# Kernel tuning notes

Measured on AMD Instinct MI355X. Metric: run time of the kernel, lower is better.

## Reference

```python
import jax, jax.numpy as jnp
import numpy as np

TEMP = 0.07
W00 = 0.1
EPS = 1e-8


def setup_inputs() -> dict:
    key = jax.random.key(0)
    k1, k2, k3, k4 = jax.random.split(key, 4)
    B, N, D = 32, 256, 256
    M = B * N
    return {
        "audio_feats": jax.random.normal(k1, (B, N, D), dtype=jnp.float32),
        "visual_feats": jax.random.normal(k2, (B, N, D), dtype=jnp.float32),
        "audio_labels": jax.random.randint(k3, (M,), 0, 2, dtype=jnp.int64)
            if jax.config.jax_enable_x64 else jax.random.randint(k3, (M,), 0, 2, dtype=jnp.int32),
        "visual_labels": jax.random.randint(k4, (M,), 0, 2, dtype=jnp.int64)
            if jax.config.jax_enable_x64 else jax.random.randint(k4, (M,), 0, 2, dtype=jnp.int32),
    }


def reference(audio_feats, visual_feats, audio_labels, visual_labels):
    B, N, D = audio_feats.shape
    M = B * N
    a = audio_feats.reshape(M, D)
    v = visual_feats.reshape(M, D)
    # L2 normalize (torch F.normalize uses eps=1e-12 clamp on norm)
    a = a / jnp.maximum(jnp.linalg.norm(a, axis=-1, keepdims=True), 1e-12)
    v = v / jnp.maximum(jnp.linalg.norm(v, axis=-1, keepdims=True), 1e-12)
    sim = (a @ v.T) / TEMP  # (M, M)
    exp_sim = jnp.exp(sim)
    la = audio_labels[:, None]  # (M, 1)
    lv = visual_labels[None, :]  # (1, M)
    pos_mask = (la == lv) & ((la == 1) | (la == 0))
    weight = jnp.where(la == 1, 1.0, W00) * pos_mask.astype(sim.dtype)  # (M, M)
    wexp = exp_sim * weight

    # audio -> visual (row direction)
    denom_a2v = exp_sim.sum(axis=1)
    num_a2v = wexp.sum(axis=1)
    frac_a2v = (num_a2v + EPS) / (denom_a2v + EPS)
    valid_a2v = (num_a2v > 0).astype(sim.dtype)
    loss_a2v = -(valid_a2v * jnp.log(frac_a2v)).sum() / jnp.maximum(valid_a2v.sum(), 1.0)

    # visual -> audio (column direction)
    denom_v2a = exp_sim.sum(axis=0)
    num_v2a = wexp.sum(axis=0)
    frac_v2a = (num_v2a + EPS) / (denom_v2a + EPS)
    valid_v2a = (num_v2a > 0).astype(sim.dtype)
    loss_v2a = -(valid_v2a * jnp.log(frac_v2a)).sum() / jnp.maximum(valid_v2a.sum(), 1.0)

    return 0.5 * (loss_a2v + loss_v2a)
```

## Files before the change

kernel.cpp:

```cpp
#include <hip/hip_runtime.h>

#define M_ROWS 8192
#define D_DIM  256
#define BM     256
#define BN     128
#define NBI    (M_ROWS / BM)
#define NBJ    (M_ROWS / BN)

#define ALPHA  4.53982478f


typedef __attribute__((ext_vector_type(8))) short  short8;
typedef __attribute__((ext_vector_type(4))) float  floatx4;

__device__ inline unsigned short f2bf(float f) {
    union { float f; unsigned int u; } v; v.f = f;
    unsigned int u = v.u;
    u = (u + 0x7fffu + ((u >> 16) & 1u)) >> 16;
    return (unsigned short)u;
}

__device__ inline float bf2f(unsigned short b) {
    union { unsigned int u; float f; } v; v.u = (unsigned int)b << 16;
    return v.f;
}

__device__ inline float fast_exp2(float x) {
#if __has_builtin(__builtin_amdgcn_exp2f)
    return __builtin_amdgcn_exp2f(x);
#else
    return exp2f(x);
#endif
}

__global__ __launch_bounds__(256) void normalize_kernel(
    const float* __restrict__ af, const float* __restrict__ vf,
    unsigned char* __restrict__ aB, unsigned char* __restrict__ vB)
{
    __shared__ unsigned short tileS[16 * 264];

    const int b = blockIdx.x;
    const bool isA = b < 512;
    const int T = isA ? b : b - 512;
    const float* src = (isA ? af : vf) + (size_t)T * 16 * D_DIM;
    unsigned char* dst = (isA ? aB : vB) + (size_t)T * 512 * 8;

    const int t = threadIdx.x;
    const int row = t >> 4, c = t & 15;

    const float* p = src + row * D_DIM + c * 16;
    float4 x0 = ((const float4*)p)[0], x1 = ((const float4*)p)[1];
    float4 x2 = ((const float4*)p)[2], x3 = ((const float4*)p)[3];
    float ss = x0.x*x0.x + x0.y*x0.y + x0.z*x0.z + x0.w*x0.w
             + x1.x*x1.x + x1.y*x1.y + x1.z*x1.z + x1.w*x1.w
             + x2.x*x2.x + x2.y*x2.y + x2.z*x2.z + x2.w*x2.w
             + x3.x*x3.x + x3.y*x3.y + x3.z*x3.z + x3.w*x3.w;
    #pragma unroll
    for (int m = 1; m < 16; m <<= 1) ss += __shfl_xor(ss, m, 64);
    float scale = ALPHA / fmaxf(sqrtf(ss), 1e-12f);

    unsigned short* q = tileS + row * 264 + c * 16;
    ushort4 o0, o1, o2, o3;
    o0.x = f2bf(x0.x*scale); o0.y = f2bf(x0.y*scale); o0.z = f2bf(x0.z*scale); o0.w = f2bf(x0.w*scale);
    o1.x = f2bf(x1.x*scale); o1.y = f2bf(x1.y*scale); o1.z = f2bf(x1.z*scale); o1.w = f2bf(x1.w*scale);
    o2.x = f2bf(x2.x*scale); o2.y = f2bf(x2.y*scale); o2.z = f2bf(x2.z*scale); o2.w = f2bf(x2.w*scale);
    o3.x = f2bf(x3.x*scale); o3.y = f2bf(x3.y*scale); o3.z = f2bf(x3.z*scale); o3.w = f2bf(x3.w*scale);
    ((ushort4*)q)[0] = o0; ((ushort4*)q)[1] = o1;
    ((ushort4*)q)[2] = o2; ((ushort4*)q)[3] = o3;
    __syncthreads();

    #pragma unroll
    for (int s = 0; s < 2; ++s) {
        const int ch  = t + s * 256;
        const int l16 = ch & 15, quad = (ch >> 4) & 3, k32 = ch >> 6;
        const unsigned short* rp = &tileS[l16 * 264 + k32 * 32 + quad * 8];
        float f0 = bf2f(rp[0]), f1 = bf2f(rp[1]), f2 = bf2f(rp[2]), f3 = bf2f(rp[3]);
        float f4 = bf2f(rp[4]), f5 = bf2f(rp[5]), f6 = bf2f(rp[6]), f7 = bf2f(rp[7]);
        int p0 = __builtin_amdgcn_cvt_pk_fp8_f32(f0, f1, 0, false);
        p0     = __builtin_amdgcn_cvt_pk_fp8_f32(f2, f3, p0, true);
        int p1 = __builtin_amdgcn_cvt_pk_fp8_f32(f4, f5, 0, false);
        p1     = __builtin_amdgcn_cvt_pk_fp8_f32(f6, f7, p1, true);
        int2 outv; outv.x = p0; outv.y = p1;
        *(int2*)(dst + (size_t)ch * 8) = outv;
    }
}

__global__ __launch_bounds__(256, 2) void gemm_loss_kernel(
    const unsigned char* __restrict__ aB, const unsigned char* __restrict__ vB,
    const int* __restrict__ la, const int* __restrict__ lv,
    float* __restrict__ rowPart, float* __restrict__ colPart)
{
    const int tid  = threadIdx.x;
    const int wave = tid >> 6, lane = tid & 63;
    const int quad = lane >> 4, l16 = lane & 15;

    const int super = blockIdx.x >> 8;
    const int inner = blockIdx.x & 255;
    const int bx = (super & 1) * 16 + (inner & 15);
    const int by = (super >> 1) * 16 + (inner >> 4);
    const int i0 = bx * BM, j0 = by * BN;

    const unsigned char* Abase = aB + ((size_t)(bx * 16 + wave * 4) * 512 + lane) * 8;
    const unsigned char* Vbase = vB + ((size_t)(by * 8) * 512 + lane) * 8;

    floatx4 acc[4][8] = {};
    long long afr[3][4], bfr[3][8];

    #pragma unroll
    for (int s = 0; s < 2; ++s) {
        #pragma unroll
        for (int it = 0; it < 4; ++it)
            afr[s][it] = *(const long long*)(Abase + it * 4096 + s * 512);
        #pragma unroll
        for (int jt = 0; jt < 8; ++jt)
            bfr[s][jt] = *(const long long*)(Vbase + jt * 4096 + s * 512);
    }

    #pragma unroll
    for (int k32 = 0; k32 < 8; ++k32) {
        const int cur = k32 % 3;
        if (k32 < 6) {
            const int nx = (k32 + 2) % 3;
            const size_t ko = (size_t)(k32 + 2) * 512;
            #pragma unroll
            for (int it = 0; it < 4; ++it)
                afr[nx][it] = *(const long long*)(Abase + it * 4096 + ko);
            #pragma unroll
            for (int jt = 0; jt < 8; ++jt)
                bfr[nx][jt] = *(const long long*)(Vbase + jt * 4096 + ko);
        }
        #pragma unroll
        for (int it = 0; it < 4; ++it)
            #pragma unroll
            for (int jt = 0; jt < 8; ++jt)
                acc[it][jt] = __builtin_amdgcn_mfma_f32_16x16x32_fp8_fp8(
                    afr[cur][it], bfr[cur][jt], acc[it][jt], 0, 0, 0);
    }

    const int baseRow = i0 + wave * 64;
    float maf[4][4];
    #pragma unroll
    for (int it = 0; it < 4; ++it)
        #pragma unroll
        for (int r = 0; r < 4; ++r)
            maf[it][r] = (float)la[baseRow + it * 16 + quad * 4 + r];
    float mvf[8];
    #pragma unroll
    for (int jt = 0; jt < 8; ++jt)
        mvf[jt] = (float)lv[j0 + jt * 16 + l16];

    float rT[4][4] = {}, r1[4][4] = {};
    float cT[8] = {}, c1[8] = {};
    #pragma unroll
    for (int it = 0; it < 4; ++it) {
        #pragma unroll
        for (int jt = 0; jt < 8; ++jt) {
            #pragma unroll
            for (int r = 0; r < 4; ++r) {
                float e = fast_exp2(acc[it][jt][r]);
                rT[it][r] += e;
                r1[it][r] = fmaf(mvf[jt], e, r1[it][r]);
                cT[jt] += e;
                c1[jt] = fmaf(maf[it][r], e, c1[jt]);
            }
        }
    }

    #pragma unroll
    for (int jt = 0; jt < 8; ++jt) {
        float t0 = cT[jt], t1 = c1[jt];
        t0 += __shfl_xor(t0, 16, 64); t0 += __shfl_xor(t0, 32, 64);
        t1 += __shfl_xor(t1, 16, 64); t1 += __shfl_xor(t1, 32, 64);
        cT[jt] = t0; c1[jt] = t1;
    }

    __shared__ float rowbuf[2 * BM];
    __shared__ float colbuf[8 * BN];

    #pragma unroll
    for (int it = 0; it < 4; ++it) {
        #pragma unroll
        for (int r = 0; r < 4; ++r) {
            float s0 = rT[it][r], s1 = r1[it][r];
            #pragma unroll
            for (int m = 1; m < 16; m <<= 1) {
                s0 += __shfl_xor(s0, m, 64);
                s1 += __shfl_xor(s1, m, 64);
            }
            if (l16 == 0) {
                int rl = wave * 64 + it * 16 + quad * 4 + r;
                rowbuf[rl * 2 + 0] = s0;
                rowbuf[rl * 2 + 1] = s1;
            }
        }
    }
    if (quad == 0) {
        #pragma unroll
        for (int jt = 0; jt < 8; ++jt) {
            colbuf[(wave * 2 + 0) * BN + jt * 16 + l16] = cT[jt];
            colbuf[(wave * 2 + 1) * BN + jt * 16 + l16] = c1[jt];
        }
    }
    __syncthreads();

    {
        *(float2*)&rowPart[((size_t)by * M_ROWS + i0 + tid) * 2] = ((float2*)rowbuf)[tid];
        const int rl  = tid >> 1;
        const int cls = tid & 1;
        float s = colbuf[(0 * 2 + cls) * BN + rl] + colbuf[(1 * 2 + cls) * BN + rl]
                + colbuf[(2 * 2 + cls) * BN + rl] + colbuf[(3 * 2 + cls) * BN + rl];
        colPart[((size_t)bx * M_ROWS + j0 + rl) * 2 + cls] = s;
    }
}

__global__ __launch_bounds__(256) void reduce_kernel(
    const float* __restrict__ rowPart, const float* __restrict__ colPart,
    const int* __restrict__ la, const int* __restrict__ lv,
    float* __restrict__ blockPart)
{
    const int bid = blockIdx.x;
    const bool aside = bid < 32;
    const int idx = (aside ? bid : bid - 32) * 256 + threadIdx.x;
    const float* part = aside ? rowPart : colPart;
    const int* lab = aside ? la : lv;
    const int nb = aside ? NBJ : NBI;

    float tot = 0.f, c1 = 0.f;
    #pragma unroll 4
    for (int b = 0; b < nb; ++b) {
        float2 p = *(const float2*)(part + ((size_t)b * M_ROWS + idx) * 2);
        tot += p.x; c1 += p.y;
    }
    float num = lab[idx] ? c1 : 0.1f * (tot - c1);
    float lg = 0.f, cnt = 0.f;
    if (num > 0.f) { lg = logf((num + 1e-8f) / (tot + 1e-8f)); cnt = 1.f; }

    #pragma unroll
    for (int m = 1; m < 64; m <<= 1) {
        lg  += __shfl_xor(lg,  m, 64);
        cnt += __shfl_xor(cnt, m, 64);
    }
    __shared__ float red[4][2];
    const int w = threadIdx.x >> 6, ln = threadIdx.x & 63;
    if (ln == 0) { red[w][0] = lg; red[w][1] = cnt; }
    __syncthreads();
    if (threadIdx.x == 0) {
        blockPart[bid * 2 + 0] = red[0][0] + red[1][0] + red[2][0] + red[3][0];
        blockPart[bid * 2 + 1] = red[0][1] + red[1][1] + red[2][1] + red[3][1];
    }
}

__global__ void finalize_kernel(const float* __restrict__ blockPart, float* __restrict__ out)
{
    const int lane = threadIdx.x & 63;
    float lg  = blockPart[lane * 2 + 0];
    float cnt = blockPart[lane * 2 + 1];
    #pragma unroll
    for (int m = 1; m < 32; m <<= 1) {
        lg  += __shfl_xor(lg,  m, 64);
        cnt += __shfl_xor(cnt, m, 64);
    }
    float sA = __shfl(lg, 0, 64),  cA = __shfl(cnt, 0, 64);
    float sV = __shfl(lg, 32, 64), cV = __shfl(cnt, 32, 64);
    if (threadIdx.x == 0) {
        float lossA = -sA / fmaxf(cA, 1.f);
        float lossV = -sV / fmaxf(cV, 1.f);
        out[0] = 0.5f * (lossA + lossV);
    }
}

extern "C" void kernel_launch(void* const* d_in, const int* in_sizes, int n_in,
                              void* d_out, int out_size, void* d_ws, size_t ws_size,
                              hipStream_t stream)
{
    const float* af = (const float*)d_in[0];
    const float* vf = (const float*)d_in[1];
    const int*   la = (const int*)d_in[2];
    const int*   lv = (const int*)d_in[3];
    float* out = (float*)d_out;

    char* ws = (char*)d_ws;
    unsigned char* aB = (unsigned char*)ws;
    unsigned char* vB = (unsigned char*)(ws + 2ull * 1024 * 1024);
    float* rowPart   = (float*)(ws +  4ull * 1024 * 1024);
    float* colPart   = (float*)(ws +  8ull * 1024 * 1024);
    float* blockPart = (float*)(ws + 10ull * 1024 * 1024);

    normalize_kernel<<<1024, 256, 0, stream>>>(af, vf, aB, vB);
    gemm_loss_kernel<<<NBI * NBJ, 256, 0, stream>>>(aB, vB, la, lv, rowPart, colPart);
    reduce_kernel<<<64, 256, 0, stream>>>(rowPart, colPart, la, lv, blockPart);
    finalize_kernel<<<1, 64, 0, stream>>>(blockPart, out);
}
```

Baseline: 136.4 us.

## Fuse all four stages into one persistent cooperative kernel with grid syncs

After: 248.8 us. +82.3%, slower.

```diff
diff --git a/kernel.cpp b/kernel.cpp
--- a/kernel.cpp
+++ b/kernel.cpp
@@ -1,4 +1,7 @@
 #include <hip/hip_runtime.h>
+#include <hip/hip_cooperative_groups.h>
+
+namespace cg = cooperative_groups;
 
 #define M_ROWS 8192
 #define D_DIM  256
@@ -6,11 +9,11 @@
 #define BN     128
 #define NBI    (M_ROWS / BM)
 #define NBJ    (M_ROWS / BN)
+#define NJOBS  (NBI * NBJ)
 
 #define ALPHA  4.53982478f
 
 
-typedef __attribute__((ext_vector_type(8))) short  short8;
 typedef __attribute__((ext_vector_type(4))) float  floatx4;
 
 __device__ inline unsigned short f2bf(float f) {
@@ -33,239 +36,238 @@
 #endif
 }
 
-__global__ __launch_bounds__(256) void normalize_kernel(
+__global__ __launch_bounds__(256, 2) void fused_kernel(
     const float* __restrict__ af, const float* __restrict__ vf,
-    unsigned char* __restrict__ aB, unsigned char* __restrict__ vB)
+    const int* __restrict__ la, const int* __restrict__ lv,
+    unsigned char* __restrict__ aB, unsigned char* __restrict__ vB,
+    float* __restrict__ rowPart, float* __restrict__ colPart,
+    float* __restrict__ blockPart, float* __restrict__ out)
 {
     __shared__ unsigned short tileS[16 * 264];
-
-    const int b = blockIdx.x;
-    const bool isA = b < 512;
-    const int T = isA ? b : b - 512;
-    const float* src = (isA ? af : vf) + (size_t)T * 16 * D_DIM;
-    unsigned char* dst = (isA ? aB : vB) + (size_t)T * 512 * 8;
-
-    const int t = threadIdx.x;
-    const int row = t >> 4, c = t & 15;
-
-    const float* p = src + row * D_DIM + c * 16;
-    float4 x0 = ((const float4*)p)[0], x1 = ((const float4*)p)[1];
-    float4 x2 = ((const float4*)p)[2], x3 = ((const float4*)p)[3];
-    float ss = x0.x*x0.x + x0.y*x0.y + x0.z*x0.z + x0.w*x0.w
-             + x1.x*x1.x + x1.y*x1.y + x1.z*x1.z + x1.w*x1.w
-             + x2.x*x2.x + x2.y*x2.y + x2.z*x2.z + x2.w*x2.w
-             + x3.x*x3.x + x3.y*x3.y + x3.z*x3.z + x3.w*x3.w;
-    #pragma unroll
-    for (int m = 1; m < 16; m <<= 1) ss += __shfl_xor(ss, m, 64);
-    float scale = ALPHA / fmaxf(sqrtf(ss), 1e-12f);
-
-    unsigned short* q = tileS + row * 264 + c * 16;
-    ushort4 o0, o1, o2, o3;
-    o0.x = f2bf(x0.x*scale); o0.y = f2bf(x0.y*scale); o0.z = f2bf(x0.z*scale); o0.w = f2bf(x0.w*scale);
-    o1.x = f2bf(x1.x*scale); o1.y = f2bf(x1.y*scale); o1.z = f2bf(x1.z*scale); o1.w = f2bf(x1.w*scale);
-    o2.x = f2bf(x2.x*scale); o2.y = f2bf(x2.y*scale); o2.z = f2bf(x2.z*scale); o2.w = f2bf(x2.w*scale);
-    o3.x = f2bf(x3.x*scale); o3.y = f2bf(x3.y*scale); o3.z = f2bf(x3.z*scale); o3.w = f2bf(x3.w*scale);
-    ((ushort4*)q)[0] = o0; ((ushort4*)q)[1] = o1;
-    ((ushort4*)q)[2] = o2; ((ushort4*)q)[3] = o3;
-    __syncthreads();
-
-    #pragma unroll
-    for (int s = 0; s < 2; ++s) {
-        const int ch  = t + s * 256;
-        const int l16 = ch & 15, quad = (ch >> 4) & 3, k32 = ch >> 6;
-        const unsigned short* rp = &tileS[l16 * 264 + k32 * 32 + quad * 8];
-        float f0 = bf2f(rp[0]), f1 = bf2f(rp[1]), f2 = bf2f(rp[2]), f3 = bf2f(rp[3]);
-        float f4 = bf2f(rp[4]), f5 = bf2f(rp[5]), f6 = bf2f(rp[6]), f7 = bf2f(rp[7]);
-        int p0 = __builtin_amdgcn_cvt_pk_fp8_f32(f0, f1, 0, false);
-        p0     = __builtin_amdgcn_cvt_pk_fp8_f32(f2, f3, p0, true);
-        int p1 = __builtin_amdgcn_cvt_pk_fp8_f32(f4, f5, 0, false);
-        p1     = __builtin_amdgcn_cvt_pk_fp8_f32(f6, f7, p1, true);
-        int2 outv; outv.x = p0; outv.y = p1;
-        *(int2*)(dst + (size_t)ch * 8) = outv;
-    }
-}
-
-__global__ __launch_bounds__(256, 2) void gemm_loss_kernel(
-    const unsigned char* __restrict__ aB, const unsigned char* __restrict__ vB,
-    const int* __restrict__ la, const int* __restrict__ lv,
-    float* __restrict__ rowPart, float* __restrict__ colPart)
-{
+    __shared__ float red[4][2];
+    cg::grid_group grid = cg::this_grid();
+
     const int tid  = threadIdx.x;
+    const int bid  = blockIdx.x;
+    const int G    = gridDim.x;
     const int wave = tid >> 6, lane = tid & 63;
     const int quad = lane >> 4, l16 = lane & 15;
 
-    const int super = blockIdx.x >> 8;
-    const int inner = blockIdx.x & 255;
-    const int bx = (super & 1) * 16 + (inner & 15);
-    const int by = (super >> 1) * 16 + (inner >> 4);
-    const int i0 = bx * BM, j0 = by * BN;
-
-    const unsigned char* Abase = aB + ((size_t)(bx * 16 + wave * 4) * 512 + lane) * 8;
-    const unsigned char* Vbase = vB + ((size_t)(by * 8) * 512 + lane) * 8;
-
-    floatx4 acc[4][8] = {};
-    long long afr[3][4], bfr[3][8];
-
-    #pragma unroll
-    for (int s = 0; s < 2; ++s) {
+    for (int u = bid; u < 1024; u += G) {
+        const bool isA = u < 512;
+        const int T = isA ? u : u - 512;
+        const float* src = (isA ? af : vf) + (size_t)T * 16 * D_DIM;
+        unsigned char* dst = (isA ? aB : vB) + (size_t)T * 4096;
+
+        const int row = tid >> 4, c = tid & 15;
+        const float* p = src + row * D_DIM + c * 16;
+        float4 x0 = ((const float4*)p)[0], x1 = ((const float4*)p)[1];
+        float4 x2 = ((const float4*)p)[2], x3 = ((const float4*)p)[3];
+        float ss = x0.x*x0.x + x0.y*x0.y + x0.z*x0.z + x0.w*x0.w
+                 + x1.x*x1.x + x1.y*x1.y + x1.z*x1.z + x1.w*x1.w
+                 + x2.x*x2.x + x2.y*x2.y + x2.z*x2.z + x2.w*x2.w
+                 + x3.x*x3.x + x3.y*x3.y + x3.z*x3.z + x3.w*x3.w;
+        #pragma unroll
+        for (int m = 1; m < 16; m <<= 1) ss += __shfl_xor(ss, m, 64);
+        float scale = ALPHA / fmaxf(sqrtf(ss), 1e-12f);
+
+        unsigned short* q = tileS + row * 264 + c * 16;
+        ushort4 o0, o1, o2, o3;
+        o0.x = f2bf(x0.x*scale); o0.y = f2bf(x0.y*scale); o0.z = f2bf(x0.z*scale); o0.w = f2bf(x0.w*scale);
+        o1.x = f2bf(x1.x*scale); o1.y = f2bf(x1.y*scale); o1.z = f2bf(x1.z*scale); o1.w = f2bf(x1.w*scale);
+        o2.x = f2bf(x2.x*scale); o2.y = f2bf(x2.y*scale); o2.z = f2bf(x2.z*scale); o2.w = f2bf(x2.w*scale);
+        o3.x = f2bf(x3.x*scale); o3.y = f2bf(x3.y*scale); o3.z = f2bf(x3.z*scale); o3.w = f2bf(x3.w*scale);
+        ((ushort4*)q)[0] = o0; ((ushort4*)q)[1] = o1;
+        ((ushort4*)q)[2] = o2; ((ushort4*)q)[3] = o3;
+        __syncthreads();
+
+        #pragma unroll
+        for (int s = 0; s < 2; ++s) {
+            const int ch  = tid + s * 256;
+            const int cl16 = ch & 15, cq = (ch >> 4) & 3, ck = ch >> 6;
+            const unsigned short* rp = &tileS[cl16 * 264 + ck * 32 + cq * 8];
+            float f0 = bf2f(rp[0]), f1 = bf2f(rp[1]), f2 = bf2f(rp[2]), f3 = bf2f(rp[3]);
+            float f4 = bf2f(rp[4]), f5 = bf2f(rp[5]), f6 = bf2f(rp[6]), f7 = bf2f(rp[7]);
+            int p0 = __builtin_amdgcn_cvt_pk_fp8_f32(f0, f1, 0, false);
+            p0     = __builtin_amdgcn_cvt_pk_fp8_f32(f2, f3, p0, true);
+            int p1 = __builtin_amdgcn_cvt_pk_fp8_f32(f4, f5, 0, false);
+            p1     = __builtin_amdgcn_cvt_pk_fp8_f32(f6, f7, p1, true);
+            int2 outv; outv.x = p0; outv.y = p1;
+            *(int2*)(dst + (size_t)ch * 8) = outv;
+        }
+        __syncthreads();
+    }
+    grid.sync();
+
+    float* rowbuf = (float*)tileS;
+    float* colbuf = (float*)tileS + 512;
+
+    for (int job = bid; job < NJOBS; job += G) {
+        const int super = job >> 8;
+        const int inner = job & 255;
+        const int bx = (super & 1) * 16 + (inner & 15);
+        const int by = (super >> 1) * 16 + (inner >> 4);
+        const int i0 = bx * BM, j0 = by * BN;
+
+        const unsigned char* Abase = aB + ((size_t)(bx * 16 + wave * 4) * 512 + lane) * 8;
+        const unsigned char* Vbase = vB + ((size_t)(by * 8) * 512 + lane) * 8;
+
+        floatx4 acc[4][8] = {};
+        long long afr[3][4], bfr[3][8];
+
+        #pragma unroll
+        for (int s = 0; s < 2; ++s) {
+            #pragma unroll
+            for (int it = 0; it < 4; ++it)
+                afr[s][it] = *(const long long*)(Abase + it * 4096 + s * 512);
+            #pragma unroll
+            for (int jt = 0; jt < 8; ++jt)
+                bfr[s][jt] = *(const long long*)(Vbase + jt * 4096 + s * 512);
+        }
+
+        #pragma unroll
+        for (int k32 = 0; k32 < 8; ++k32) {
+            const int cur = k32 % 3;
+            if (k32 < 6) {
+                const int nx = (k32 + 2) % 3;
+                const size_t ko = (size_t)(k32 + 2) * 512;
+                #pragma unroll
+                for (int it = 0; it < 4; ++it)
+                    afr[nx][it] = *(const long long*)(Abase + it * 4096 + ko);
+                #pragma unroll
+                for (int jt = 0; jt < 8; ++jt)
+                    bfr[nx][jt] = *(const long long*)(Vbase + jt * 4096 + ko);
+            }
+            #pragma unroll
+            for (int it = 0; it < 4; ++it)
+                #pragma unroll
+                for (int jt = 0; jt < 8; ++jt)
+                    acc[it][jt] = __builtin_amdgcn_mfma_f32_16x16x32_fp8_fp8(
+                        afr[cur][it], bfr[cur][jt], acc[it][jt], 0, 0, 0);
+        }
+
+        const int baseRow = i0 + wave * 64;
+        float maf[4][4];
         #pragma unroll
         for (int it = 0; it < 4; ++it)
-            afr[s][it] = *(const long long*)(Abase + it * 4096 + s * 512);
+            #pragma unroll
+            for (int r = 0; r < 4; ++r)
+                maf[it][r] = (float)la[baseRow + it * 16 + quad * 4 + r];
+        float mvf[8];
         #pragma unroll
         for (int jt = 0; jt < 8; ++jt)
-            bfr[s][jt] = *(const long long*)(Vbase + jt * 4096 + s * 512);
+            mvf[jt] = (float)lv[j0 + jt * 16 + l16];
+
+        float rT[4][4] = {}, r1[4][4] = {};
+        float cT[8] = {}, c1[8] = {};
+        #pragma unroll
+        for (int it = 0; it < 4; ++it) {
+            #pragma unroll
+            for (int jt = 0; jt < 8; ++jt) {
+                #pragma unroll
+                for (int r = 0; r < 4; ++r) {
+                    float e = fast_exp2(acc[it][jt][r]);
+                    rT[it][r] += e;
+                    r1[it][r] = fmaf(mvf[jt], e, r1[it][r]);
+                    cT[jt] += e;
+                    c1[jt] = fmaf(maf[it][r], e, c1[jt]);
+                }
+            }
+        }
+
+        #pragma unroll
+        for (int jt = 0; jt < 8; ++jt) {
+            float t0 = cT[jt], t1 = c1[jt];
+            t0 += __shfl_xor(t0, 16, 64); t0 += __shfl_xor(t0, 32, 64);
+            t1 += __shfl_xor(t1, 16, 64); t1 += __shfl_xor(t1, 32, 64);
+            cT[jt] = t0; c1[jt] = t1;
+        }
+
+        #pragma unroll
+        for (int it = 0; it < 4; ++it) {
+            #pragma unroll
+            for (int r = 0; r < 4; ++r) {
+                float s0 = rT[it][r], s1 = r1[it][r];
+                #pragma unroll
+                for (int m = 1; m < 16; m <<= 1) {
+                    s0 += __shfl_xor(s0, m, 64);
+                    s1 += __shfl_xor(s1, m, 64);
+                }
+                if (l16 == 0) {
+                    int rl = wave * 64 + it * 16 + quad * 4 + r;
+                    rowbuf[rl * 2 + 0] = s0;
+                    rowbuf[rl * 2 + 1] = s1;
+                }
+            }
+        }
+        if (quad == 0) {
+            #pragma unroll
+            for (int jt = 0; jt < 8; ++jt) {
+                colbuf[(wave * 2 + 0) * BN + jt * 16 + l16] = cT[jt];
+                colbuf[(wave * 2 + 1) * BN + jt * 16 + l16] = c1[jt];
+            }
+        }
+        __syncthreads();
+
+        *(float2*)&rowPart[((size_t)by * M_ROWS + i0 + tid) * 2] = ((float2*)rowbuf)[tid];
+        {
+            const int rl  = tid >> 1;
+            const int cls = tid & 1;
+            float s = colbuf[(0 * 2 + cls) * BN + rl] + colbuf[(1 * 2 + cls) * BN + rl]
+                    + colbuf[(2 * 2 + cls) * BN + rl] + colbuf[(3 * 2 + cls) * BN + rl];
+            colPart[((size_t)bx * M_ROWS + j0 + rl) * 2 + cls] = s;
+        }
+        __syncthreads();
     }
-
-    #pragma unroll
-    for (int k32 = 0; k32 < 8; ++k32) {
-        const int cur = k32 % 3;
-        if (k32 < 6) {
-            const int nx = (k32 + 2) % 3;
-            const size_t ko = (size_t)(k32 + 2) * 512;
-            #pragma unroll
-            for (int it = 0; it < 4; ++it)
-                afr[nx][it] = *(const long long*)(Abase + it * 4096 + ko);
-            #pragma unroll
-            for (int jt = 0; jt < 8; ++jt)
-                bfr[nx][jt] = *(const long long*)(Vbase + jt * 4096 + ko);
-        }
-        #pragma unroll
-        for (int it = 0; it < 4; ++it)
-            #pragma unroll
-            for (int jt = 0; jt < 8; ++jt)
-                acc[it][jt] = __builtin_amdgcn_mfma_f32_16x16x32_fp8_fp8(
-                    afr[cur][it], bfr[cur][jt], acc[it][jt], 0, 0, 0);
+    grid.sync();
+
+    for (int rb = bid; rb < 64; rb += G) {
+        const bool aside = rb < 32;
+        const int idx = (aside ? rb : rb - 32) * 256 + tid;
+        const float* part = aside ? rowPart : colPart;
+        const int* lab = aside ? la : lv;
+        const int nb = aside ? NBJ : NBI;
+
+        float tot = 0.f, c1 = 0.f;
+        #pragma unroll 4
+        for (int b = 0; b < nb; ++b) {
+            float2 p = *(const float2*)(part + ((size_t)b * M_ROWS + idx) * 2);
+            tot += p.x; c1 += p.y;
+        }
+        float num = lab[idx] ? c1 : 0.1f * (tot - c1);
+        float lg = 0.f, cnt = 0.f;
+        if (num > 0.f) { lg = logf((num + 1e-8f) / (tot + 1e-8f)); cnt = 1.f; }
+
+        #pragma unroll
+        for (int m = 1; m < 64; m <<= 1) {
+            lg  += __shfl_xor(lg,  m, 64);
+            cnt += __shfl_xor(cnt, m, 64);
+        }
+        if (lane == 0) { red[wave][0] = lg; red[wave][1] = cnt; }
+        __syncthreads();
+        if (tid == 0) {
+            blockPart[rb * 2 + 0] = red[0][0] + red[1][0] + red[2][0] + red[3][0];
+            blockPart[rb * 2 + 1] = red[0][1] + red[1][1] + red[2][1] + red[3][1];
+        }
+        __syncthreads();
     }
-
-    const int baseRow = i0 + wave * 64;
-    float maf[4][4];
-    #pragma unroll
-    for (int it = 0; it < 4; ++it)
-        #pragma unroll
-        for (int r = 0; r < 4; ++r)
-            maf[it][r] = (float)la[baseRow + it * 16 + quad * 4 + r];
-    float mvf[8];
-    #pragma unroll
-    for (int jt = 0; jt < 8; ++jt)
-        mvf[jt] = (float)lv[j0 + jt * 16 + l16];
-
-    float rT[4][4] = {}, r1[4][4] = {};
-    float cT[8] = {}, c1[8] = {};
-    #pragma unroll
-    for (int it = 0; it < 4; ++it) {
-        #pragma unroll
-        for (int jt = 0; jt < 8; ++jt) {
-            #pragma unroll
-            for (int r = 0; r < 4; ++r) {
-                float e = fast_exp2(acc[it][jt][r]);
-                rT[it][r] += e;
-                r1[it][r] = fmaf(mvf[jt], e, r1[it][r]);
-                cT[jt] += e;
-                c1[jt] = fmaf(maf[it][r], e, c1[jt]);
-            }
-        }
-    }
-
-    #pragma unroll
-    for (int jt = 0; jt < 8; ++jt) {
-        float t0 = cT[jt], t1 = c1[jt];
-        t0 += __shfl_xor(t0, 16, 64); t0 += __shfl_xor(t0, 32, 64);
-        t1 += __shfl_xor(t1, 16, 64); t1 += __shfl_xor(t1, 32, 64);
-        cT[jt] = t0; c1[jt] = t1;
-    }
-
-    __shared__ float rowbuf[2 * BM];
-    __shared__ float colbuf[8 * BN];
-
-    #pragma unroll
-    for (int it = 0; it < 4; ++it) {
-        #pragma unroll
-        for (int r = 0; r < 4; ++r) {
-            float s0 = rT[it][r], s1 = r1[it][r];
-            #pragma unroll
-            for (int m = 1; m < 16; m <<= 1) {
-                s0 += __shfl_xor(s0, m, 64);
-                s1 += __shfl_xor(s1, m, 64);
-            }
-            if (l16 == 0) {
-                int rl = wave * 64 + it * 16 + quad * 4 + r;
-                rowbuf[rl * 2 + 0] = s0;
-                rowbuf[rl * 2 + 1] = s1;
-            }
-        }
-    }
-    if (quad == 0) {
-        #pragma unroll
-        for (int jt = 0; jt < 8; ++jt) {
-            colbuf[(wave * 2 + 0) * BN + jt * 16 + l16] = cT[jt];
-            colbuf[(wave * 2 + 1) * BN + jt * 16 + l16] = c1[jt];
-        }
-    }
-    __syncthreads();
-
-    {
-        *(float2*)&rowPart[((size_t)by * M_ROWS + i0 + tid) * 2] = ((float2*)rowbuf)[tid];
-        const int rl  = tid >> 1;
-        const int cls = tid & 1;
-        float s = colbuf[(0 * 2 + cls) * BN + rl] + colbuf[(1 * 2 + cls) * BN + rl]
-                + colbuf[(2 * 2 + cls) * BN + rl] + colbuf[(3 * 2 + cls) * BN + rl];
-        colPart[((size_t)bx * M_ROWS + j0 + rl) * 2 + cls] = s;
-    }
-}
-
-__global__ __launch_bounds__(256) void reduce_kernel(
-    const float* __restrict__ rowPart, const float* __restrict__ colPart,
-    const int* __restrict__ la, const int* __restrict__ lv,
-    float* __restrict__ blockPart)
-{
-    const int bid = blockIdx.x;
-    const bool aside = bid < 32;
-    const int idx = (aside ? bid : bid - 32) * 256 + threadIdx.x;
-    const float* part = aside ? rowPart : colPart;
-    const int* lab = aside ? la : lv;
-    const int nb = aside ? NBJ : NBI;
-
-    float tot = 0.f, c1 = 0.f;
-    #pragma unroll 4
-    for (int b = 0; b < nb; ++b) {
-        float2 p = *(const float2*)(part + ((size_t)b * M_ROWS + idx) * 2);
-        tot += p.x; c1 += p.y;
-    }
-    float num = lab[idx] ? c1 : 0.1f * (tot - c1);
-    float lg = 0.f, cnt = 0.f;
-    if (num > 0.f) { lg = logf((num + 1e-8f) / (tot + 1e-8f)); cnt = 1.f; }
-
-    #pragma unroll
-    for (int m = 1; m < 64; m <<= 1) {
-        lg  += __shfl_xor(lg,  m, 64);
-        cnt += __shfl_xor(cnt, m, 64);
-    }
-    __shared__ float red[4][2];
-    const int w = threadIdx.x >> 6, ln = threadIdx.x & 63;
-    if (ln == 0) { red[w][0] = lg; red[w][1] = cnt; }
-    __syncthreads();
-    if (threadIdx.x == 0) {
-        blockPart[bid * 2 + 0] = red[0][0] + red[1][0] + red[2][0] + red[3][0];
-        blockPart[bid * 2 + 1] = red[0][1] + red[1][1] + red[2][1] + red[3][1];
-    }
-}
-
-__global__ void finalize_kernel(const float* __restrict__ blockPart, float* __restrict__ out)
-{
-    const int lane = threadIdx.x & 63;
-    float lg  = blockPart[lane * 2 + 0];
-    float cnt = blockPart[lane * 2 + 1];
-    #pragma unroll
-    for (int m = 1; m < 32; m <<= 1) {
-        lg  += __shfl_xor(lg,  m, 64);
-        cnt += __shfl_xor(cnt, m, 64);
-    }
-    float sA = __shfl(lg, 0, 64),  cA = __shfl(cnt, 0, 64);
-    float sV = __shfl(lg, 32, 64), cV = __shfl(cnt, 32, 64);
-    if (threadIdx.x == 0) {
-        float lossA = -sA / fmaxf(cA, 1.f);
-        float lossV = -sV / fmaxf(cV, 1.f);
-        out[0] = 0.5f * (lossA + lossV);
+    grid.sync();
+
+    if (bid == 0 && tid < 64) {
+        float lg  = blockPart[tid * 2 + 0];
+        float cnt = blockPart[tid * 2 + 1];
+        #pragma unroll
+        for (int m = 1; m < 32; m <<= 1) {
+            lg  += __shfl_xor(lg,  m, 64);
+            cnt += __shfl_xor(cnt, m, 64);
+        }
+        float sA = __shfl(lg, 0, 64),  cA = __shfl(cnt, 0, 64);
+        float sV = __shfl(lg, 32, 64), cV = __shfl(cnt, 32, 64);
+        if (tid == 0) {
+            float lossA = -sA / fmaxf(cA, 1.f);
+            float lossV = -sV / fmaxf(cV, 1.f);
+            out[0] = 0.5f * (lossA + lossV);
+        }
     }
 }
 
@@ -286,8 +288,15 @@
     float* colPart   = (float*)(ws +  8ull * 1024 * 1024);
     float* blockPart = (float*)(ws + 10ull * 1024 * 1024);
 
-    normalize_kernel<<<1024, 256, 0, stream>>>(af, vf, aB, vB);
-    gemm_loss_kernel<<<NBI * NBJ, 256, 0, stream>>>(aB, vB, la, lv, rowPart, colPart);
-    reduce_kernel<<<64, 256, 0, stream>>>(rowPart, colPart, la, lv, blockPart);
-    finalize_kernel<<<1, 64, 0, stream>>>(blockPart, out);
-}
+    int nb = 0;
+    hipOccupancyMaxActiveBlocksPerMultiprocessor(&nb, fused_kernel, 256, 0);
+    if (nb < 1) nb = 1;
+    long long g = (long long)nb * 256;
+    if (g > 512) g = 512;
+
+    void* args[] = { (void*)&af, (void*)&vf, (void*)&la, (void*)&lv,
+                     (void*)&aB, (void*)&vB, (void*)&rowPart, (void*)&colPart,
+                     (void*)&blockPart, (void*)&out };
+    hipLaunchCooperativeKernel((void*)fused_kernel, dim3((unsigned)g), dim3(256),
+                               args, 0, stream);
+}
```

## Halve GEMM row tile to 128 and fold finalize into reduce via atomics

Applied to the files above, without the earlier changes.

Measured after the change: 130.4 us. 4.4% less time.

```diff
diff --git a/kernel.cpp b/kernel.cpp
--- a/kernel.cpp
+++ b/kernel.cpp
@@ -2,15 +2,15 @@
 
 #define M_ROWS 8192
 #define D_DIM  256
-#define BM     256
+#define BM     128
 #define BN     128
 #define NBI    (M_ROWS / BM)
 #define NBJ    (M_ROWS / BN)
+#define NJOBS  (NBI * NBJ)
 
 #define ALPHA  4.53982478f
 
 
-typedef __attribute__((ext_vector_type(8))) short  short8;
 typedef __attribute__((ext_vector_type(4))) float  floatx4;
 
 __device__ inline unsigned short f2bf(float f) {
@@ -35,15 +35,21 @@
 
 __global__ __launch_bounds__(256) void normalize_kernel(
     const float* __restrict__ af, const float* __restrict__ vf,
-    unsigned char* __restrict__ aB, unsigned char* __restrict__ vB)
+    unsigned char* __restrict__ aB, unsigned char* __restrict__ vB,
+    float* __restrict__ glob)
 {
     __shared__ unsigned short tileS[16 * 264];
+
+    if (blockIdx.x == 0) {
+        if (threadIdx.x < 4) glob[threadIdx.x] = 0.f;
+        if (threadIdx.x == 4) ((int*)glob)[4] = 0;
+    }
 
     const int b = blockIdx.x;
     const bool isA = b < 512;
     const int T = isA ? b : b - 512;
     const float* src = (isA ? af : vf) + (size_t)T * 16 * D_DIM;
-    unsigned char* dst = (isA ? aB : vB) + (size_t)T * 512 * 8;
+    unsigned char* dst = (isA ? aB : vB) + (size_t)T * 4096;
 
     const int t = threadIdx.x;
     const int row = t >> 4, c = t & 15;
@@ -85,7 +91,7 @@
     }
 }
 
-__global__ __launch_bounds__(256, 2) void gemm_loss_kernel(
+__global__ __launch_bounds__(256, 3) void gemm_loss_kernel(
     const unsigned char* __restrict__ aB, const unsigned char* __restrict__ vB,
     const int* __restrict__ la, const int* __restrict__ lv,
     float* __restrict__ rowPart, float* __restrict__ colPart)
@@ -96,20 +102,20 @@
 
     const int super = blockIdx.x >> 8;
     const int inner = blockIdx.x & 255;
-    const int bx = (super & 1) * 16 + (inner & 15);
-    const int by = (super >> 1) * 16 + (inner >> 4);
+    const int bx = (super & 3) * 16 + (inner & 15);
+    const int by = (super >> 2) * 16 + (inner >> 4);
     const int i0 = bx * BM, j0 = by * BN;
 
-    const unsigned char* Abase = aB + ((size_t)(bx * 16 + wave * 4) * 512 + lane) * 8;
+    const unsigned char* Abase = aB + ((size_t)(bx * 8 + wave * 2) * 512 + lane) * 8;
     const unsigned char* Vbase = vB + ((size_t)(by * 8) * 512 + lane) * 8;
 
-    floatx4 acc[4][8] = {};
-    long long afr[3][4], bfr[3][8];
+    floatx4 acc[2][8] = {};
+    long long afr[3][2], bfr[3][8];
 
     #pragma unroll
     for (int s = 0; s < 2; ++s) {
         #pragma unroll
-        for (int it = 0; it < 4; ++it)
+        for (int it = 0; it < 2; ++it)
             afr[s][it] = *(const long long*)(Abase + it * 4096 + s * 512);
         #pragma unroll
         for (int jt = 0; jt < 8; ++jt)
@@ -123,24 +129,24 @@
             const int nx = (k32 + 2) % 3;
             const size_t ko = (size_t)(k32 + 2) * 512;
             #pragma unroll
-            for (int it = 0; it < 4; ++it)
+            for (int it = 0; it < 2; ++it)
                 afr[nx][it] = *(const long long*)(Abase + it * 4096 + ko);
             #pragma unroll
             for (int jt = 0; jt < 8; ++jt)
                 bfr[nx][jt] = *(const long long*)(Vbase + jt * 4096 + ko);
         }
         #pragma unroll
-        for (int it = 0; it < 4; ++it)
+        for (int it = 0; it < 2; ++it)
             #pragma unroll
             for (int jt = 0; jt < 8; ++jt)
                 acc[it][jt] = __builtin_amdgcn_mfma_f32_16x16x32_fp8_fp8(
                     afr[cur][it], bfr[cur][jt], acc[it][jt], 0, 0, 0);
     }
 
-    const int baseRow = i0 + wave * 64;
-    float maf[4][4];
-    #pragma unroll
-    for (int it = 0; it < 4; ++it)
+    const int baseRow = i0 + wave * 32;
+    float maf[2][4];
+    #pragma unroll
+    for (int it = 0; it < 2; ++it)
         #pragma unroll
         for (int r = 0; r < 4; ++r)
             maf[it][r] = (float)la[baseRow + it * 16 + quad * 4 + r];
@@ -149,10 +155,10 @@
     for (int jt = 0; jt < 8; ++jt)
         mvf[jt] = (float)lv[j0 + jt * 16 + l16];
 
-    float rT[4][4] = {}, r1[4][4] = {};
+    float rT[2][4] = {}, r1[2][4] = {};
     float cT[8] = {}, c1[8] = {};
     #pragma unroll
-    for (int it = 0; it < 4; ++it) {
+    for (int it = 0; it < 2; ++it) {
         #pragma unroll
         for (int jt = 0; jt < 8; ++jt) {
             #pragma unroll
@@ -178,7 +184,7 @@
     __shared__ float colbuf[8 * BN];
 
     #pragma unroll
-    for (int it = 0; it < 4; ++it) {
+    for (int it = 0; it < 2; ++it) {
         #pragma unroll
         for (int r = 0; r < 4; ++r) {
             float s0 = rT[it][r], s1 = r1[it][r];
@@ -188,7 +194,7 @@
                 s1 += __shfl_xor(s1, m, 64);
             }
             if (l16 == 0) {
-                int rl = wave * 64 + it * 16 + quad * 4 + r;
+                int rl = wave * 32 + it * 16 + quad * 4 + r;
                 rowbuf[rl * 2 + 0] = s0;
                 rowbuf[rl * 2 + 1] = s1;
             }
@@ -204,9 +210,9 @@
     __syncthreads();
 
     {
-        *(float2*)&rowPart[((size_t)by * M_ROWS + i0 + tid) * 2] = ((float2*)rowbuf)[tid];
         const int rl  = tid >> 1;
         const int cls = tid & 1;
+        rowPart[((size_t)by * M_ROWS + i0 + rl) * 2 + cls] = rowbuf[rl * 2 + cls];
         float s = colbuf[(0 * 2 + cls) * BN + rl] + colbuf[(1 * 2 + cls) * BN + rl]
                 + colbuf[(2 * 2 + cls) * BN + rl] + colbuf[(3 * 2 + cls) * BN + rl];
         colPart[((size_t)bx * M_ROWS + j0 + rl) * 2 + cls] = s;
@@ -216,18 +222,17 @@
 __global__ __launch_bounds__(256) void reduce_kernel(
     const float* __restrict__ rowPart, const float* __restrict__ colPart,
     const int* __restrict__ la, const int* __restrict__ lv,
-    float* __restrict__ blockPart)
+    float* __restrict__ glob, float* __restrict__ out)
 {
     const int bid = blockIdx.x;
     const bool aside = bid < 32;
     const int idx = (aside ? bid : bid - 32) * 256 + threadIdx.x;
     const float* part = aside ? rowPart : colPart;
     const int* lab = aside ? la : lv;
-    const int nb = aside ? NBJ : NBI;
 
     float tot = 0.f, c1 = 0.f;
     #pragma unroll 4
-    for (int b = 0; b < nb; ++b) {
+    for (int b = 0; b < 64; ++b) {
         float2 p = *(const float2*)(part + ((size_t)b * M_ROWS + idx) * 2);
         tot += p.x; c1 += p.y;
     }
@@ -245,27 +250,23 @@
     if (ln == 0) { red[w][0] = lg; red[w][1] = cnt; }
     __syncthreads();
     if (threadIdx.x == 0) {
-        blockPart[bid * 2 + 0] = red[0][0] + red[1][0] + red[2][0] + red[3][0];
-        blockPart[bid * 2 + 1] = red[0][1] + red[1][1] + red[2][1] + red[3][1];
-    }
-}
-
-__global__ void finalize_kernel(const float* __restrict__ blockPart, float* __restrict__ out)
-{
-    const int lane = threadIdx.x & 63;
-    float lg  = blockPart[lane * 2 + 0];
-    float cnt = blockPart[lane * 2 + 1];
-    #pragma unroll
-    for (int m = 1; m < 32; m <<= 1) {
-        lg  += __shfl_xor(lg,  m, 64);
-        cnt += __shfl_xor(cnt, m, 64);
-    }
-    float sA = __shfl(lg, 0, 64),  cA = __shfl(cnt, 0, 64);
-    float sV = __shfl(lg, 32, 64), cV = __shfl(cnt, 32, 64);
-    if (threadIdx.x == 0) {
-        float lossA = -sA / fmaxf(cA, 1.f);
-        float lossV = -sV / fmaxf(cV, 1.f);
-        out[0] = 0.5f * (lossA + lossV);
+        float slg  = red[0][0] + red[1][0] + red[2][0] + red[3][0];
+        float scnt = red[0][1] + red[1][1] + red[2][1] + red[3][1];
+        float* base = glob + (aside ? 0 : 2);
+        atomicAdd(&base[0], slg);
+        atomicAdd(&base[1], scnt);
+        __threadfence();
+        int old = atomicAdd((int*)glob + 4, 1);
+        if (old == 63) {
+            __threadfence();
+            float sA = atomicAdd(&glob[0], 0.f);
+            float cA = atomicAdd(&glob[1], 0.f);
+            float sV = atomicAdd(&glob[2], 0.f);
+            float cV = atomicAdd(&glob[3], 0.f);
+            float lossA = -sA / fmaxf(cA, 1.f);
+            float lossV = -sV / fmaxf(cV, 1.f);
+            out[0] = 0.5f * (lossA + lossV);
+        }
     }
 }
 
@@ -284,10 +285,9 @@
     unsigned char* vB = (unsigned char*)(ws + 2ull * 1024 * 1024);
     float* rowPart   = (float*)(ws +  4ull * 1024 * 1024);
     float* colPart   = (float*)(ws +  8ull * 1024 * 1024);
-    float* blockPart = (float*)(ws + 10ull * 1024 * 1024);
-
-    normalize_kernel<<<1024, 256, 0, stream>>>(af, vf, aB, vB);
-    gemm_loss_kernel<<<NBI * NBJ, 256, 0, stream>>>(aB, vB, la, lv, rowPart, colPart);
-    reduce_kernel<<<64, 256, 0, stream>>>(rowPart, colPart, la, lv, blockPart);
-    finalize_kernel<<<1, 64, 0, stream>>>(blockPart, out);
-}
+    float* glob      = (float*)(ws + 12ull * 1024 * 1024);
+
+    normalize_kernel<<<1024, 256, 0, stream>>>(af, vf, aB, vB, glob);
+    gemm_loss_kernel<<<NJOBS, 256, 0, stream>>>(aB, vB, la, lv, rowPart, colPart);
+    reduce_kernel<<<64, 256, 0, stream>>>(rowPart, colPart, la, lv, glob, out);
+}
```
